# Kernel tuning notes

Hardware: AMD Instinct MI355X
Metric: run time of the kernel (lower is better)

The kernel has to match this reference:

```python
import jax, jax.numpy as jnp
import numpy as np

SIMPLE_W = 1.0
NON_SIMPLE_W = 5.0

# connectivity offset sets (exclude center)
_ALL26 = [(a, b, c) for a in (-1, 0, 1) for b in (-1, 0, 1) for c in (-1, 0, 1) if (a, b, c) != (0, 0, 0)]
OFF6 = [o for o in _ALL26 if abs(o[0]) + abs(o[1]) + abs(o[2]) == 1]          # scipy default structure
OFF18 = [o for o in _ALL26 if not (abs(o[0]) == 1 and abs(o[1]) == 1 and abs(o[2]) == 1)]  # the 's' structure
OFF26 = _ALL26                                                                  # np.ones((3,3,3))


def global_label(fg):
    """Connected-component labels (6-connectivity) via max-propagation.
    Labels are distinct positive ints per component (values differ from scipy's
    1..K but only label *equality* is used downstream). fg: bool [D,H,W]."""
    D, H, W = fg.shape
    idx = (jnp.arange(fg.size, dtype=jnp.int32) + 1).reshape(fg.shape)
    lab0 = jnp.where(fg, idx, 0)

    def step(lab):
        p = jnp.pad(lab, 1)
        m = lab
        for dz, dy, dx in OFF6:
            m = jnp.maximum(m, p[1 + dz:1 + dz + D, 1 + dy:1 + dy + H, 1 + dx:1 + dx + W])
        return jnp.where(fg, m, 0)

    def cond(c):
        return ~c[1]

    def body(c):
        lab, _ = c
        new = step(lab)
        return new, jnp.all(new == lab)

    lab, _ = jax.lax.while_loop(cond, body, (lab0, jnp.array(False)))
    return lab


def local_ncomp(mask, offsets):
    """Number of connected components inside each 3x3x3 window.
    mask: bool [N,3,3,3]. Max-propagation of unique seeds for 26 iters
    (>= max path length among 27 voxels); a component is counted where the
    surviving max label equals its own seed."""
    seed = (jnp.arange(27, dtype=jnp.int32) + 1).reshape(3, 3, 3)
    lab0 = jnp.where(mask, seed, 0)

    def body(_, lab):
        p = jnp.pad(lab, ((0, 0), (1, 1), (1, 1), (1, 1)))
        m = lab
        for dz, dy, dx in offsets:
            m = jnp.maximum(m, p[:, 1 + dz:4 + dz, 1 + dy:4 + dy, 1 + dx:4 + dx])
        return jnp.where(mask, m, 0)

    lab = jax.lax.fori_loop(0, 26, body, lab0)
    return jnp.sum((lab == seed) & mask, axis=(1, 2, 3))


def nonsimple_map(x):
    """Per-voxel non-simple-point indicator, float, same shape as x."""
    D, H, W = x.shape
    fg = x > 0
    glab = global_label(fg)
    p = jnp.pad(glab, 1, mode='edge')  # np.pad(..., 'edge')
    # 3x3x3 label windows per voxel -> [N,3,3,3]
    wins = jnp.stack([p[dz:dz + D, dy:dy + H, dx:dx + W]
                      for dz in range(3) for dy in range(3) for dx in range(3)], axis=-1)
    wins = wins.reshape(-1, 3, 3, 3)
    center = wins[:, 1, 1, 1]  # [N]
    c = center[:, None, None, None]
    # test 1: complement-of-center-label components (18-connectivity) must be exactly 1
    n1 = local_ncomp(wins != c, OFF18)
    # test 2: center-label components with center voxel removed (26-conn) must be exactly 1
    mask2 = (wins == c).at[:, 1, 1, 1].set(False)
    n2 = local_ncomp(mask2, OFF26)
    ns = (center != 0) & ((n1 != 1) | (n2 != 1))
    return ns.reshape(D, H, W).astype(x.dtype)


def setup_inputs() -> dict:
    key = jax.random.key(0)
    k1, k2 = jax.random.split(key)
    D = H = W = 64
    prediction = jax.random.normal(k1, (D, H, W), dtype=jnp.float32)
    label = jax.random.randint(k2, (D, H, W), 0, 2).astype(jnp.float32)
    return {"prediction": prediction, "label": label}


def reference(prediction, label):
    pw = nonsimple_map(prediction)
    lw = nonsimple_map(label)
    w_bool = (pw + lw) > 0
    weight = jnp.where(w_bool, NON_SIMPLE_W, SIMPLE_W).astype(prediction.dtype)
    # BCEWithLogitsLoss(reduction='none'): max(x,0) - x*y + log(1+exp(-|x|))
    cost = jnp.maximum(prediction, 0.0) - prediction * label + jnp.log1p(jnp.exp(-jnp.abs(prediction)))
    return jnp.mean(weight * cost)
```

## Files before the change

kernel.cpp:

```cpp
#include <hip/hip_runtime.h>

#define DIM 64
#define NVOX (DIM * DIM * DIM)
#define EPF 53248

__device__ __forceinline__ int find_root_link(int* L, int v) {
    for (;;) {
        int p = L[v];
        if (p == v) return v;
        int gp = L[p];
        if (gp == p) return p;
        L[v] = gp;
        v = gp;
    }
}

__device__ __forceinline__ void unite(int* L, int a, int b) {
    int ra = find_root_link(L, a);
    int rb = find_root_link(L, b);
    while (ra != rb) {
        if (ra > rb) { int t = ra; ra = rb; rb = t; }
        int old = atomicCAS(&L[rb], rb, ra);
        if (old == rb) break;
        rb = find_root_link(L, old);
        ra = find_root_link(L, ra);
    }
}

__device__ __forceinline__ int chase(const int* __restrict__ L, int p) {
    int q = L[p];
    while (q != p) { p = q; q = L[p]; }
    return p;
}

__global__ void local_ccl(const float* __restrict__ pred,
                          const float* __restrict__ lab,
                          int* __restrict__ LP, int* __restrict__ LL,
                          float* __restrict__ out) {
    __shared__ int s_lab[2048];
    int t = threadIdx.x;
    if (blockIdx.x == 0 && blockIdx.y == 0 && t == 0) *out = 0.0f;
    int b = blockIdx.x;
    int tx = b & 3, ty = (b >> 2) & 3, tz = b >> 4;
    int X0 = tx << 4, Y0 = ty << 4, Z0 = tz << 3;

    const float* src = blockIdx.y ? lab : pred;
    int* Lg = blockIdx.y ? LL : LP;

    bool fg[8];
    int vv[8];
#pragma unroll
    for (int i = 0; i < 8; ++i) {
        int l = t + (i << 8);
        int v = ((Z0 + (l >> 8)) << 12) | ((Y0 + ((l >> 4) & 15)) << 6)
              | (X0 + (l & 15));
        vv[i] = v;
        fg[i] = src[v] > 0.0f;
        s_lab[l] = fg[i] ? l : -1;
    }
    __syncthreads();

#pragma unroll
    for (int i = 0; i < 8; ++i) {
        if (!fg[i]) continue;
        int l = t + (i << 8);
        int lx = l & 15, ly = (l >> 4) & 15, lz = l >> 8;
        if (lx < 15 && s_lab[l + 1]   >= 0) unite(s_lab, l, l + 1);
        if (ly < 15 && s_lab[l + 16]  >= 0) unite(s_lab, l, l + 16);
        if (lz < 7  && s_lab[l + 256] >= 0) unite(s_lab, l, l + 256);
    }
    __syncthreads();

#pragma unroll
    for (int i = 0; i < 8; ++i) {
        int g = -1;
        if (fg[i]) {
            int p = s_lab[t + (i << 8)];
            while (s_lab[p] != p) p = s_lab[p];
            g = ((Z0 + (p >> 8)) << 12) | ((Y0 + ((p >> 4) & 15)) << 6)
              | (X0 + (p & 15));
        }
        Lg[vv[i]] = g;
    }
}

__global__ void boundary_link(int* __restrict__ LP, int* __restrict__ LL) {
    int r = blockIdx.x * blockDim.x + threadIdx.x;
    int v, n;
    if (r < 12288) {
        int plane = 15 + ((r >> 12) << 4);
        int ij = r & 4095;
        v = ((ij >> 6) << 12) | ((ij & 63) << 6) | plane;
        n = v + 1;
    } else if (r < 24576) {
        int r2 = r - 12288;
        int plane = 15 + ((r2 >> 12) << 4);
        int ij = r2 & 4095;
        v = ((ij >> 6) << 12) | (plane << 6) | (ij & 63);
        n = v + 64;
    } else {
        int r3 = r - 24576;
        int plane = 7 + ((r3 >> 12) << 3);
        int ij = r3 & 4095;
        v = (plane << 12) | ((ij >> 6) << 6) | (ij & 63);
        n = v + 4096;
    }

    int lane = threadIdx.x & 63;

    int pa = LP[v], pb = LP[n];
    int la = LL[v], lb = LL[n];
    bool doP = (pa >= 0) & (pb >= 0);
    bool doL = (la >= 0) & (lb >= 0);

    int xpa = __shfl_up(pa, 1, 64), xpb = __shfl_up(pb, 1, 64);
    int xla = __shfl_up(la, 1, 64), xlb = __shfl_up(lb, 1, 64);
    if (lane && xpa == pa && xpb == pb) doP = false;
    if (lane && xla == la && xlb == lb) doL = false;

    int rp0 = -1, rp1 = -1, rl0 = -1, rl1 = -1;
    if (doP) {
        int u0 = chase(LP, pa), u1 = chase(LP, pb);
        rp0 = min(u0, u1); rp1 = max(u0, u1);
    }
    if (doL) {
        int u0 = chase(LL, la), u1 = chase(LL, lb);
        rl0 = min(u0, u1); rl1 = max(u0, u1);
    }

    int qp0 = __shfl_up(rp0, 1, 64), qp1 = __shfl_up(rp1, 1, 64);
    int ql0 = __shfl_up(rl0, 1, 64), ql1 = __shfl_up(rl1, 1, 64);
    bool dupP = lane && (qp0 == rp0) && (qp1 == rp1);
    bool dupL = lane && (ql0 == rl0) && (ql1 == rl1);

    if (rp0 >= 0 && rp0 != rp1 && !dupP) unite(LP, rp0, rp1);
    if (rl0 >= 0 && rl0 != rl1 && !dupL) unite(LL, rl0, rl1);
}

#define MX_L 0x6DB6DB6u
#define MX_R 0x36DB6DBu
#define MY_L 0x7E3F1F8u
#define MY_R 0x0FC7E3Fu
#define M27  0x7FFFFFFu

__device__ __forceinline__ unsigned dil26(unsigned m) {
    m |= ((m << 1) & MX_L) | ((m >> 1) & MX_R);
    m |= ((m << 3) & MY_L) | ((m >> 3) & MY_R);
    m |= ((m << 9) & M27)  | (m >> 9);
    return m;
}
__device__ __forceinline__ unsigned dil18(unsigned m) {
    unsigned ax = m | ((m << 1) & MX_L) | ((m >> 1) & MX_R);
    unsigned ay = m | ((m << 3) & MY_L) | ((m >> 3) & MY_R);
    unsigned dxy = ax | ((ax << 3) & MY_L) | ((ax >> 3) & MY_R);
    unsigned dxz = ax | ((ax << 9) & M27)  | (ax >> 9);
    unsigned dyz = ay | ((ay << 9) & M27)  | (ay >> 9);
    return dxy | dxz | dyz;
}

__device__ __forceinline__ bool single18(unsigned m) {
    if (!m) return false;
    unsigned c = m & (~m + 1u);
    for (;;) {
        unsigned n = dil18(c) & m;
        if (n == m) return true;
        if (n == c) return false;
        c = n;
    }
}
__device__ __forceinline__ bool single26(unsigned m) {
    if (!m) return false;
    unsigned c = m & (~m + 1u);
    for (;;) {
        unsigned n = dil26(c) & m;
        if (n == m) return true;
        if (n == c) return false;
        c = n;
    }
}

#define HV 1000

__global__ void finalize_kernel(const float* __restrict__ pred,
                                const float* __restrict__ lab,
                                const int* __restrict__ LP,
                                const int* __restrict__ LL,
                                float* __restrict__ out) {
    __shared__ int sP[HV], sL[HV];
    __shared__ float s_part[4];
    int t = threadIdx.x;
    int b = blockIdx.x;
    int rx = b & 7, ry = (b >> 3) & 7, rz = b >> 6;
    int x0 = rx << 3, y0 = ry << 3, z0 = rz << 3;

    int pv[4], lv[4];
#pragma unroll
    for (int j = 0; j < 4; ++j) {
        int i = t + (j << 8);
        if (i < HV) {
            int hx = i % 10, rr = i / 10, hy = rr % 10, hz = rr / 10;
            int gx = x0 + hx - 1; gx = gx < 0 ? 0 : (gx > 63 ? 63 : gx);
            int gy = y0 + hy - 1; gy = gy < 0 ? 0 : (gy > 63 ? 63 : gy);
            int gz = z0 + hz - 1; gz = gz < 0 ? 0 : (gz > 63 ? 63 : gz);
            int gv = (gz << 12) | (gy << 6) | gx;
            pv[j] = LP[gv];
            lv[j] = LL[gv];
        }
    }
#pragma unroll
    for (int j = 0; j < 4; ++j) {
        int i = t + (j << 8);
        if (i < HV) {
            int p = pv[j];
            if (p >= 0) p = chase(LP, p);
            sP[i] = p;
            p = lv[j];
            if (p >= 0) p = chase(LL, p);
            sL[i] = p;
        }
    }
    __syncthreads();

    float acc = 0.0f;
#pragma unroll
    for (int j = 0; j < 2; ++j) {
        int l = t + (j << 8);
        int lx = l & 7, ly = (l >> 3) & 7, lz = l >> 6;
        int x = x0 | lx, y = y0 | ly, z = z0 | lz;
        int v = (z << 12) | (y << 6) | x;
        int base = lz * 100 + ly * 10 + lx;

        bool nsP = false, nsL = false;
        {
            int c = sP[base + 111];
            if (c >= 0) {
                unsigned m1 = 0, m2 = 0; int k = 0;
#pragma unroll
                for (int kz = 0; kz < 3; ++kz)
#pragma unroll
                    for (int ky = 0; ky < 3; ++ky)
#pragma unroll
                        for (int kx = 0; kx < 3; ++kx, ++k) {
                            int w = sP[base + kz * 100 + ky * 10 + kx];
                            m1 |= (unsigned)(w != c) << k;
                            m2 |= (unsigned)(w == c) << k;
                        }
                m2 &= ~(1u << 13);
                nsP = !(single18(m1) && single26(m2));
            }
        }
        {
            int c = sL[base + 111];
            if (c >= 0) {
                unsigned m1 = 0, m2 = 0; int k = 0;
#pragma unroll
                for (int kz = 0; kz < 3; ++kz)
#pragma unroll
                    for (int ky = 0; ky < 3; ++ky)
#pragma unroll
                        for (int kx = 0; kx < 3; ++kx, ++k) {
                            int w = sL[base + kz * 100 + ky * 10 + kx];
                            m1 |= (unsigned)(w != c) << k;
                            m2 |= (unsigned)(w == c) << k;
                        }
                m2 &= ~(1u << 13);
                nsL = !(single18(m1) && single26(m2));
            }
        }

        float p = pred[v], lvf = lab[v];
        float cost = fmaxf(p, 0.0f) - p * lvf + log1pf(__expf(-fabsf(p)));
        acc += ((nsP || nsL) ? 5.0f : 1.0f) * cost;
    }

#pragma unroll
    for (int off = 32; off > 0; off >>= 1)
        acc += __shfl_down(acc, off, 64);
    if ((t & 63) == 0) s_part[t >> 6] = acc;
    __syncthreads();
    if (t == 0) {
        float s = s_part[0] + s_part[1] + s_part[2] + s_part[3];
        atomicAdd(out, s * (1.0f / (float)NVOX));
    }
}

extern "C" void kernel_launch(void* const* d_in, const int* in_sizes, int n_in,
                              void* d_out, int out_size, void* d_ws, size_t ws_size,
                              hipStream_t stream) {
    const float* pred = (const float*)d_in[0];
    const float* lab  = (const float*)d_in[1];
    float* out = (float*)d_out;

    int* LP = (int*)d_ws;
    int* LL = LP + NVOX;

    hipLaunchKernelGGL(local_ccl, dim3(128, 2), dim3(256), 0, stream,
                       pred, lab, LP, LL, out);
    hipLaunchKernelGGL(boundary_link, dim3(EPF / 256), dim3(256), 0, stream,
                       LP, LL);
    hipLaunchKernelGGL(finalize_kernel, dim3(512), dim3(256), 0, stream,
                       pred, lab, LP, LL, out);
}
```

Measured before the change: 110.0 us.

## Fuse three CCL kernels into one cooperative kernel with grid syncs

Merges local tile labeling, boundary linking and the finalize/loss pass into a single cooperative launch of 512 blocks, separated by grid-wide barriers, and reuses one shared-memory union for the tile and halo buffers. The local labeling phase also switches to float4/int4 vectorized loads and stores with 4 consecutive voxels per thread. The goal is to remove two kernel launch gaps. In exchange, every phase now runs at 512 blocks, which is idle capacity for the 256-block labeling phase, and it adds grid.sync overhead and a dependence on all blocks being co-resident.

```diff
diff --git a/kernel.cpp b/kernel.cpp
--- a/kernel.cpp
+++ b/kernel.cpp
@@ -1,8 +1,12 @@
 #include <hip/hip_runtime.h>
+#include <hip/hip_cooperative_groups.h>
+
+namespace cg = cooperative_groups;
 
 #define DIM 64
 #define NVOX (DIM * DIM * DIM)
 #define EPF 53248
+#define HV 1000
 
 __device__ __forceinline__ int find_root_link(int* L, int v) {
     for (;;) {
@@ -33,110 +37,6 @@
     return p;
 }
 
-__global__ void local_ccl(const float* __restrict__ pred,
-                          const float* __restrict__ lab,
-                          int* __restrict__ LP, int* __restrict__ LL,
-                          float* __restrict__ out) {
-    __shared__ int s_lab[2048];
-    int t = threadIdx.x;
-    if (blockIdx.x == 0 && blockIdx.y == 0 && t == 0) *out = 0.0f;
-    int b = blockIdx.x;
-    int tx = b & 3, ty = (b >> 2) & 3, tz = b >> 4;
-    int X0 = tx << 4, Y0 = ty << 4, Z0 = tz << 3;
-
-    const float* src = blockIdx.y ? lab : pred;
-    int* Lg = blockIdx.y ? LL : LP;
-
-    bool fg[8];
-    int vv[8];
-#pragma unroll
-    for (int i = 0; i < 8; ++i) {
-        int l = t + (i << 8);
-        int v = ((Z0 + (l >> 8)) << 12) | ((Y0 + ((l >> 4) & 15)) << 6)
-              | (X0 + (l & 15));
-        vv[i] = v;
-        fg[i] = src[v] > 0.0f;
-        s_lab[l] = fg[i] ? l : -1;
-    }
-    __syncthreads();
-
-#pragma unroll
-    for (int i = 0; i < 8; ++i) {
-        if (!fg[i]) continue;
-        int l = t + (i << 8);
-        int lx = l & 15, ly = (l >> 4) & 15, lz = l >> 8;
-        if (lx < 15 && s_lab[l + 1]   >= 0) unite(s_lab, l, l + 1);
-        if (ly < 15 && s_lab[l + 16]  >= 0) unite(s_lab, l, l + 16);
-        if (lz < 7  && s_lab[l + 256] >= 0) unite(s_lab, l, l + 256);
-    }
-    __syncthreads();
-
-#pragma unroll
-    for (int i = 0; i < 8; ++i) {
-        int g = -1;
-        if (fg[i]) {
-            int p = s_lab[t + (i << 8)];
-            while (s_lab[p] != p) p = s_lab[p];
-            g = ((Z0 + (p >> 8)) << 12) | ((Y0 + ((p >> 4) & 15)) << 6)
-              | (X0 + (p & 15));
-        }
-        Lg[vv[i]] = g;
-    }
-}
-
-__global__ void boundary_link(int* __restrict__ LP, int* __restrict__ LL) {
-    int r = blockIdx.x * blockDim.x + threadIdx.x;
-    int v, n;
-    if (r < 12288) {
-        int plane = 15 + ((r >> 12) << 4);
-        int ij = r & 4095;
-        v = ((ij >> 6) << 12) | ((ij & 63) << 6) | plane;
-        n = v + 1;
-    } else if (r < 24576) {
-        int r2 = r - 12288;
-        int plane = 15 + ((r2 >> 12) << 4);
-        int ij = r2 & 4095;
-        v = ((ij >> 6) << 12) | (plane << 6) | (ij & 63);
-        n = v + 64;
-    } else {
-        int r3 = r - 24576;
-        int plane = 7 + ((r3 >> 12) << 3);
-        int ij = r3 & 4095;
-        v = (plane << 12) | ((ij >> 6) << 6) | (ij & 63);
-        n = v + 4096;
-    }
-
-    int lane = threadIdx.x & 63;
-
-    int pa = LP[v], pb = LP[n];
-    int la = LL[v], lb = LL[n];
-    bool doP = (pa >= 0) & (pb >= 0);
-    bool doL = (la >= 0) & (lb >= 0);
-
-    int xpa = __shfl_up(pa, 1, 64), xpb = __shfl_up(pb, 1, 64);
-    int xla = __shfl_up(la, 1, 64), xlb = __shfl_up(lb, 1, 64);
-    if (lane && xpa == pa && xpb == pb) doP = false;
-    if (lane && xla == la && xlb == lb) doL = false;
-
-    int rp0 = -1, rp1 = -1, rl0 = -1, rl1 = -1;
-    if (doP) {
-        int u0 = chase(LP, pa), u1 = chase(LP, pb);
-        rp0 = min(u0, u1); rp1 = max(u0, u1);
-    }
-    if (doL) {
-        int u0 = chase(LL, la), u1 = chase(LL, lb);
-        rl0 = min(u0, u1); rl1 = max(u0, u1);
-    }
-
-    int qp0 = __shfl_up(rp0, 1, 64), qp1 = __shfl_up(rp1, 1, 64);
-    int ql0 = __shfl_up(rl0, 1, 64), ql1 = __shfl_up(rl1, 1, 64);
-    bool dupP = lane && (qp0 == rp0) && (qp1 == rp1);
-    bool dupL = lane && (ql0 == rl0) && (ql1 == rl1);
-
-    if (rp0 >= 0 && rp0 != rp1 && !dupP) unite(LP, rp0, rp1);
-    if (rl0 >= 0 && rl0 != rl1 && !dupL) unite(LL, rl0, rl1);
-}
-
 #define MX_L 0x6DB6DB6u
 #define MX_R 0x36DB6DBu
 #define MY_L 0x7E3F1F8u
@@ -179,108 +79,232 @@
     }
 }
 
-#define HV 1000
-
-__global__ void finalize_kernel(const float* __restrict__ pred,
-                                const float* __restrict__ lab,
-                                const int* __restrict__ LP,
-                                const int* __restrict__ LL,
-                                float* __restrict__ out) {
-    __shared__ int sP[HV], sL[HV];
+__global__ __launch_bounds__(256, 2)
+void fused_all(const float* __restrict__ pred, const float* __restrict__ lab,
+               int* __restrict__ LP, int* __restrict__ LL,
+               float* __restrict__ out) {
+    __shared__ union {
+        int tile[2048];
+        struct { int P[HV]; int L[HV]; } h;
+    } sm;
     __shared__ float s_part[4];
-    int t = threadIdx.x;
-    int b = blockIdx.x;
-    int rx = b & 7, ry = (b >> 3) & 7, rz = b >> 6;
-    int x0 = rx << 3, y0 = ry << 3, z0 = rz << 3;
-
-    int pv[4], lv[4];
-#pragma unroll
-    for (int j = 0; j < 4; ++j) {
-        int i = t + (j << 8);
-        if (i < HV) {
-            int hx = i % 10, rr = i / 10, hy = rr % 10, hz = rr / 10;
-            int gx = x0 + hx - 1; gx = gx < 0 ? 0 : (gx > 63 ? 63 : gx);
-            int gy = y0 + hy - 1; gy = gy < 0 ? 0 : (gy > 63 ? 63 : gy);
-            int gz = z0 + hz - 1; gz = gz < 0 ? 0 : (gz > 63 ? 63 : gz);
-            int gv = (gz << 12) | (gy << 6) | gx;
-            pv[j] = LP[gv];
-            lv[j] = LL[gv];
-        }
-    }
-#pragma unroll
-    for (int j = 0; j < 4; ++j) {
-        int i = t + (j << 8);
-        if (i < HV) {
-            int p = pv[j];
-            if (p >= 0) p = chase(LP, p);
-            sP[i] = p;
-            p = lv[j];
-            if (p >= 0) p = chase(LL, p);
-            sL[i] = p;
-        }
-    }
-    __syncthreads();
-
-    float acc = 0.0f;
-#pragma unroll
-    for (int j = 0; j < 2; ++j) {
-        int l = t + (j << 8);
-        int lx = l & 7, ly = (l >> 3) & 7, lz = l >> 6;
-        int x = x0 | lx, y = y0 | ly, z = z0 | lz;
-        int v = (z << 12) | (y << 6) | x;
-        int base = lz * 100 + ly * 10 + lx;
-
-        bool nsP = false, nsL = false;
-        {
-            int c = sP[base + 111];
-            if (c >= 0) {
-                unsigned m1 = 0, m2 = 0; int k = 0;
-#pragma unroll
-                for (int kz = 0; kz < 3; ++kz)
-#pragma unroll
-                    for (int ky = 0; ky < 3; ++ky)
-#pragma unroll
-                        for (int kx = 0; kx < 3; ++kx, ++k) {
-                            int w = sP[base + kz * 100 + ky * 10 + kx];
-                            m1 |= (unsigned)(w != c) << k;
-                            m2 |= (unsigned)(w == c) << k;
-                        }
-                m2 &= ~(1u << 13);
-                nsP = !(single18(m1) && single26(m2));
-            }
-        }
-        {
-            int c = sL[base + 111];
-            if (c >= 0) {
-                unsigned m1 = 0, m2 = 0; int k = 0;
-#pragma unroll
-                for (int kz = 0; kz < 3; ++kz)
-#pragma unroll
-                    for (int ky = 0; ky < 3; ++ky)
-#pragma unroll
-                        for (int kx = 0; kx < 3; ++kx, ++k) {
-                            int w = sL[base + kz * 100 + ky * 10 + kx];
-                            m1 |= (unsigned)(w != c) << k;
-                            m2 |= (unsigned)(w == c) << k;
-                        }
-                m2 &= ~(1u << 13);
-                nsL = !(single18(m1) && single26(m2));
-            }
-        }
-
-        float p = pred[v], lvf = lab[v];
-        float cost = fmaxf(p, 0.0f) - p * lvf + log1pf(__expf(-fabsf(p)));
-        acc += ((nsP || nsL) ? 5.0f : 1.0f) * cost;
-    }
-
-#pragma unroll
-    for (int off = 32; off > 0; off >>= 1)
-        acc += __shfl_down(acc, off, 64);
-    if ((t & 63) == 0) s_part[t >> 6] = acc;
-    __syncthreads();
-    if (t == 0) {
-        float s = s_part[0] + s_part[1] + s_part[2] + s_part[3];
-        atomicAdd(out, s * (1.0f / (float)NVOX));
+
+    cg::grid_group grid = cg::this_grid();
+    const int t = threadIdx.x;
+    const int b = blockIdx.x;
+
+    if (b == 0 && t == 0) *out = 0.0f;
+
+    if (b < 256) {
+        int tile = b & 127, field = b >> 7;
+        int tx = tile & 3, ty = (tile >> 2) & 3, tz = tile >> 4;
+        int X0 = tx << 4, Y0 = ty << 4, Z0 = tz << 3;
+        const float* src = field ? lab : pred;
+        int* Lg = field ? LL : LP;
+
+        bool fg[8];
+        int vbase[2];
+#pragma unroll
+        for (int j = 0; j < 2; ++j) {
+            int l0 = (j << 10) | (t << 2);
+            int lx = l0 & 15, ly = (l0 >> 4) & 15, lz = l0 >> 8;
+            int v0 = ((Z0 + lz) << 12) | ((Y0 + ly) << 6) | (X0 + lx);
+            vbase[j] = v0;
+            const float4 f = *reinterpret_cast<const float4*>(src + v0);
+            int4 s;
+            fg[j * 4 + 0] = f.x > 0.0f; s.x = fg[j * 4 + 0] ? l0 + 0 : -1;
+            fg[j * 4 + 1] = f.y > 0.0f; s.y = fg[j * 4 + 1] ? l0 + 1 : -1;
+            fg[j * 4 + 2] = f.z > 0.0f; s.z = fg[j * 4 + 2] ? l0 + 2 : -1;
+            fg[j * 4 + 3] = f.w > 0.0f; s.w = fg[j * 4 + 3] ? l0 + 3 : -1;
+            *reinterpret_cast<int4*>(&sm.tile[l0]) = s;
+        }
+        __syncthreads();
+
+#pragma unroll
+        for (int j = 0; j < 2; ++j) {
+#pragma unroll
+            for (int k = 0; k < 4; ++k) {
+                if (!fg[j * 4 + k]) continue;
+                int l = ((j << 10) | (t << 2)) + k;
+                int lx = l & 15, ly = (l >> 4) & 15, lz = l >> 8;
+                if (lx < 15 && sm.tile[l + 1]   >= 0) unite(sm.tile, l, l + 1);
+                if (ly < 15 && sm.tile[l + 16]  >= 0) unite(sm.tile, l, l + 16);
+                if (lz < 7  && sm.tile[l + 256] >= 0) unite(sm.tile, l, l + 256);
+            }
+        }
+        __syncthreads();
+
+#pragma unroll
+        for (int j = 0; j < 2; ++j) {
+            int l0 = (j << 10) | (t << 2);
+            int rr[4];
+#pragma unroll
+            for (int k = 0; k < 4; ++k) {
+                int g = -1;
+                if (fg[j * 4 + k]) {
+                    int p = sm.tile[l0 + k];
+                    while (sm.tile[p] != p) p = sm.tile[p];
+                    g = ((Z0 + (p >> 8)) << 12) | ((Y0 + ((p >> 4) & 15)) << 6)
+                      | (X0 + (p & 15));
+                }
+                rr[k] = g;
+            }
+            *reinterpret_cast<int4*>(Lg + vbase[j]) =
+                make_int4(rr[0], rr[1], rr[2], rr[3]);
+        }
+    }
+
+    grid.sync();
+
+    {
+        int e = (b << 8) | t;
+        if (e < EPF) {
+            int v, n;
+            if (e < 12288) {
+                int plane = 15 + ((e >> 12) << 4);
+                int ij = e & 4095;
+                v = ((ij >> 6) << 12) | ((ij & 63) << 6) | plane;
+                n = v + 1;
+            } else if (e < 24576) {
+                int e2 = e - 12288;
+                int plane = 15 + ((e2 >> 12) << 4);
+                int ij = e2 & 4095;
+                v = ((ij >> 6) << 12) | (plane << 6) | (ij & 63);
+                n = v + 64;
+            } else {
+                int e3 = e - 24576;
+                int plane = 7 + ((e3 >> 12) << 3);
+                int ij = e3 & 4095;
+                v = (plane << 12) | ((ij >> 6) << 6) | (ij & 63);
+                n = v + 4096;
+            }
+
+            int lane = t & 63;
+            int pa = LP[v], pb = LP[n];
+            int la = LL[v], lb = LL[n];
+            bool doP = (pa >= 0) & (pb >= 0);
+            bool doL = (la >= 0) & (lb >= 0);
+
+            int xpa = __shfl_up(pa, 1, 64), xpb = __shfl_up(pb, 1, 64);
+            int xla = __shfl_up(la, 1, 64), xlb = __shfl_up(lb, 1, 64);
+            if (lane && xpa == pa && xpb == pb) doP = false;
+            if (lane && xla == la && xlb == lb) doL = false;
+
+            int rp0 = -1, rp1 = -1, rl0 = -1, rl1 = -1;
+            if (doP) {
+                int u0 = chase(LP, pa), u1 = chase(LP, pb);
+                rp0 = min(u0, u1); rp1 = max(u0, u1);
+            }
+            if (doL) {
+                int u0 = chase(LL, la), u1 = chase(LL, lb);
+                rl0 = min(u0, u1); rl1 = max(u0, u1);
+            }
+
+            int qp0 = __shfl_up(rp0, 1, 64), qp1 = __shfl_up(rp1, 1, 64);
+            int ql0 = __shfl_up(rl0, 1, 64), ql1 = __shfl_up(rl1, 1, 64);
+            bool dupP = lane && (qp0 == rp0) && (qp1 == rp1);
+            bool dupL = lane && (ql0 == rl0) && (ql1 == rl1);
+
+            if (rp0 >= 0 && rp0 != rp1 && !dupP) unite(LP, rp0, rp1);
+            if (rl0 >= 0 && rl0 != rl1 && !dupL) unite(LL, rl0, rl1);
+        }
+    }
+
+    grid.sync();
+
+    {
+        int rx = b & 7, ry = (b >> 3) & 7, rz = b >> 6;
+        int x0 = rx << 3, y0 = ry << 3, z0 = rz << 3;
+
+        int pv[4], lv[4];
+#pragma unroll
+        for (int j = 0; j < 4; ++j) {
+            int i = t + (j << 8);
+            if (i < HV) {
+                int hx = i % 10, rr = i / 10, hy = rr % 10, hz = rr / 10;
+                int gx = x0 + hx - 1; gx = gx < 0 ? 0 : (gx > 63 ? 63 : gx);
+                int gy = y0 + hy - 1; gy = gy < 0 ? 0 : (gy > 63 ? 63 : gy);
+                int gz = z0 + hz - 1; gz = gz < 0 ? 0 : (gz > 63 ? 63 : gz);
+                int gv = (gz << 12) | (gy << 6) | gx;
+                pv[j] = LP[gv];
+                lv[j] = LL[gv];
+            }
+        }
+#pragma unroll
+        for (int j = 0; j < 4; ++j) {
+            int i = t + (j << 8);
+            if (i < HV) {
+                int p = pv[j];
+                if (p >= 0) p = chase(LP, p);
+                sm.h.P[i] = p;
+                p = lv[j];
+                if (p >= 0) p = chase(LL, p);
+                sm.h.L[i] = p;
+            }
+        }
+        __syncthreads();
+
+        float acc = 0.0f;
+#pragma unroll
+        for (int j = 0; j < 2; ++j) {
+            int l = t + (j << 8);
+            int lx = l & 7, ly = (l >> 3) & 7, lz = l >> 6;
+            int x = x0 | lx, y = y0 | ly, z = z0 | lz;
+            int v = (z << 12) | (y << 6) | x;
+            int base = lz * 100 + ly * 10 + lx;
+
+            bool nsP = false, nsL = false;
+            {
+                int c = sm.h.P[base + 111];
+                if (c >= 0) {
+                    unsigned m1 = 0, m2 = 0; int k = 0;
+#pragma unroll
+                    for (int kz = 0; kz < 3; ++kz)
+#pragma unroll
+                        for (int ky = 0; ky < 3; ++ky)
+#pragma unroll
+                            for (int kx = 0; kx < 3; ++kx, ++k) {
+                                int w = sm.h.P[base + kz * 100 + ky * 10 + kx];
+                                m1 |= (unsigned)(w != c) << k;
+                                m2 |= (unsigned)(w == c) << k;
+                            }
+                    m2 &= ~(1u << 13);
+                    nsP = !(single18(m1) && single26(m2));
+                }
+            }
+            {
+                int c = sm.h.L[base + 111];
+                if (c >= 0) {
+                    unsigned m1 = 0, m2 = 0; int k = 0;
+#pragma unroll
+                    for (int kz = 0; kz < 3; ++kz)
+#pragma unroll
+                        for (int ky = 0; ky < 3; ++ky)
+#pragma unroll
+                            for (int kx = 0; kx < 3; ++kx, ++k) {
+                                int w = sm.h.L[base + kz * 100 + ky * 10 + kx];
+                                m1 |= (unsigned)(w != c) << k;
+                                m2 |= (unsigned)(w == c) << k;
+                            }
+                    m2 &= ~(1u << 13);
+                    nsL = !(single18(m1) && single26(m2));
+                }
+            }
+
+            float p = pred[v], lvf = lab[v];
+            float cost = fmaxf(p, 0.0f) - p * lvf + log1pf(__expf(-fabsf(p)));
+            acc += ((nsP || nsL) ? 5.0f : 1.0f) * cost;
+        }
+
+#pragma unroll
+        for (int off = 32; off > 0; off >>= 1)
+            acc += __shfl_down(acc, off, 64);
+        if ((t & 63) == 0) s_part[t >> 6] = acc;
+        __syncthreads();
+        if (t == 0) {
+            float s = s_part[0] + s_part[1] + s_part[2] + s_part[3];
+            atomicAdd(out, s * (1.0f / (float)NVOX));
+        }
     }
 }
 
@@ -294,10 +318,8 @@
     int* LP = (int*)d_ws;
     int* LL = LP + NVOX;
 
-    hipLaunchKernelGGL(local_ccl, dim3(128, 2), dim3(256), 0, stream,
-                       pred, lab, LP, LL, out);
-    hipLaunchKernelGGL(boundary_link, dim3(EPF / 256), dim3(256), 0, stream,
-                       LP, LL);
-    hipLaunchKernelGGL(finalize_kernel, dim3(512), dim3(256), 0, stream,
-                       pred, lab, LP, LL, out);
-}
+    void* args[] = { (void*)&pred, (void*)&lab, (void*)&LP, (void*)&LL,
+                     (void*)&out };
+    hipLaunchCooperativeKernel((const void*)fused_all, dim3(512), dim3(256),
+                               args, 0, stream);
+}
```

Result: slower. 222.5 us (+102.3%).

## Add flatten pass, vectorize local CCL, halve finalize tile depth

Applied to the files above, without the earlier changes.

Local CCL now runs 512 threads per block, each handling 4 consecutive voxels with float4 loads and int4 stores instead of 8 strided voxels. A new flatten kernel compresses every union-find label to its root once, so finalize no longer chases roots for its halo. Finalize uses 8x8x4 tiles (600-entry halo, 1024 blocks, one voxel per thread) to raise parallelism. The cost is an extra kernel launch and a full pass over both label arrays, plus more redundant halo loads overall.

```diff
diff --git a/kernel.cpp b/kernel.cpp
--- a/kernel.cpp
+++ b/kernel.cpp
@@ -33,10 +33,11 @@
     return p;
 }
 
-__global__ void local_ccl(const float* __restrict__ pred,
-                          const float* __restrict__ lab,
-                          int* __restrict__ LP, int* __restrict__ LL,
-                          float* __restrict__ out) {
+__global__ __launch_bounds__(512)
+void local_ccl(const float* __restrict__ pred,
+               const float* __restrict__ lab,
+               int* __restrict__ LP, int* __restrict__ LL,
+               float* __restrict__ out) {
     __shared__ int s_lab[2048];
     int t = threadIdx.x;
     if (blockIdx.x == 0 && blockIdx.y == 0 && t == 0) *out = 0.0f;
@@ -47,23 +48,26 @@
     const float* src = blockIdx.y ? lab : pred;
     int* Lg = blockIdx.y ? LL : LP;
 
-    bool fg[8];
-    int vv[8];
-#pragma unroll
-    for (int i = 0; i < 8; ++i) {
-        int l = t + (i << 8);
-        int v = ((Z0 + (l >> 8)) << 12) | ((Y0 + ((l >> 4) & 15)) << 6)
-              | (X0 + (l & 15));
-        vv[i] = v;
-        fg[i] = src[v] > 0.0f;
-        s_lab[l] = fg[i] ? l : -1;
+    int l0 = t << 2;
+    int lx0 = l0 & 15, ly0 = (l0 >> 4) & 15, lz0 = l0 >> 8;
+    int v0 = ((Z0 + lz0) << 12) | ((Y0 + ly0) << 6) | (X0 + lx0);
+
+    bool fg[4];
+    {
+        const float4 f = *reinterpret_cast<const float4*>(src + v0);
+        int4 s;
+        fg[0] = f.x > 0.0f; s.x = fg[0] ? l0 + 0 : -1;
+        fg[1] = f.y > 0.0f; s.y = fg[1] ? l0 + 1 : -1;
+        fg[2] = f.z > 0.0f; s.z = fg[2] ? l0 + 2 : -1;
+        fg[3] = f.w > 0.0f; s.w = fg[3] ? l0 + 3 : -1;
+        *reinterpret_cast<int4*>(&s_lab[l0]) = s;
     }
     __syncthreads();
 
 #pragma unroll
-    for (int i = 0; i < 8; ++i) {
-        if (!fg[i]) continue;
-        int l = t + (i << 8);
+    for (int k = 0; k < 4; ++k) {
+        if (!fg[k]) continue;
+        int l = l0 + k;
         int lx = l & 15, ly = (l >> 4) & 15, lz = l >> 8;
         if (lx < 15 && s_lab[l + 1]   >= 0) unite(s_lab, l, l + 1);
         if (ly < 15 && s_lab[l + 16]  >= 0) unite(s_lab, l, l + 16);
@@ -71,20 +75,25 @@
     }
     __syncthreads();
 
-#pragma unroll
-    for (int i = 0; i < 8; ++i) {
-        int g = -1;
-        if (fg[i]) {
-            int p = s_lab[t + (i << 8)];
-            while (s_lab[p] != p) p = s_lab[p];
-            g = ((Z0 + (p >> 8)) << 12) | ((Y0 + ((p >> 4) & 15)) << 6)
-              | (X0 + (p & 15));
-        }
-        Lg[vv[i]] = g;
-    }
-}
-
-__global__ void boundary_link(int* __restrict__ LP, int* __restrict__ LL) {
+    {
+        int rr[4];
+#pragma unroll
+        for (int k = 0; k < 4; ++k) {
+            int g = -1;
+            if (fg[k]) {
+                int p = s_lab[l0 + k];
+                while (s_lab[p] != p) p = s_lab[p];
+                g = ((Z0 + (p >> 8)) << 12) | ((Y0 + ((p >> 4) & 15)) << 6)
+                  | (X0 + (p & 15));
+            }
+            rr[k] = g;
+        }
+        *reinterpret_cast<int4*>(Lg + v0) = make_int4(rr[0], rr[1], rr[2], rr[3]);
+    }
+}
+
+__global__ __launch_bounds__(256)
+void boundary_link(int* __restrict__ LP, int* __restrict__ LL) {
     int r = blockIdx.x * blockDim.x + threadIdx.x;
     int v, n;
     if (r < 12288) {
@@ -137,6 +146,18 @@
     if (rl0 >= 0 && rl0 != rl1 && !dupL) unite(LL, rl0, rl1);
 }
 
+__global__ __launch_bounds__(256)
+void flatten(int* __restrict__ LP, int* __restrict__ LL) {
+    int idx = blockIdx.x * blockDim.x + threadIdx.x;
+    int* L = (idx < NVOX) ? LP : LL;
+    int i = idx & (NVOX - 1);
+    int p = L[i];
+    if (p >= 0) {
+        int r = chase(L, p);
+        if (r != p) L[i] = r;
+    }
+}
+
 #define MX_L 0x6DB6DB6u
 #define MX_R 0x36DB6DBu
 #define MY_L 0x7E3F1F8u
@@ -179,25 +200,26 @@
     }
 }
 
-#define HV 1000
-
-__global__ void finalize_kernel(const float* __restrict__ pred,
-                                const float* __restrict__ lab,
-                                const int* __restrict__ LP,
-                                const int* __restrict__ LL,
-                                float* __restrict__ out) {
-    __shared__ int sP[HV], sL[HV];
+#define HV2 600
+
+__global__ __launch_bounds__(256, 4)
+void finalize_kernel(const float* __restrict__ pred,
+                     const float* __restrict__ lab,
+                     const int* __restrict__ LP,
+                     const int* __restrict__ LL,
+                     float* __restrict__ out) {
+    __shared__ int sP[HV2], sL[HV2];
     __shared__ float s_part[4];
     int t = threadIdx.x;
     int b = blockIdx.x;
     int rx = b & 7, ry = (b >> 3) & 7, rz = b >> 6;
-    int x0 = rx << 3, y0 = ry << 3, z0 = rz << 3;
-
-    int pv[4], lv[4];
-#pragma unroll
-    for (int j = 0; j < 4; ++j) {
+    int x0 = rx << 3, y0 = ry << 3, z0 = rz << 2;
+
+    int pv[3], lv[3];
+#pragma unroll
+    for (int j = 0; j < 3; ++j) {
         int i = t + (j << 8);
-        if (i < HV) {
+        if (i < HV2) {
             int hx = i % 10, rr = i / 10, hy = rr % 10, hz = rr / 10;
             int gx = x0 + hx - 1; gx = gx < 0 ? 0 : (gx > 63 ? 63 : gx);
             int gy = y0 + hy - 1; gy = gy < 0 ? 0 : (gy > 63 ? 63 : gy);
@@ -208,23 +230,18 @@
         }
     }
 #pragma unroll
-    for (int j = 0; j < 4; ++j) {
+    for (int j = 0; j < 3; ++j) {
         int i = t + (j << 8);
-        if (i < HV) {
-            int p = pv[j];
-            if (p >= 0) p = chase(LP, p);
-            sP[i] = p;
-            p = lv[j];
-            if (p >= 0) p = chase(LL, p);
-            sL[i] = p;
+        if (i < HV2) {
+            sP[i] = pv[j];
+            sL[i] = lv[j];
         }
     }
     __syncthreads();
 
-    float acc = 0.0f;
-#pragma unroll
-    for (int j = 0; j < 2; ++j) {
-        int l = t + (j << 8);
+    float acc;
+    {
+        int l = t;
         int lx = l & 7, ly = (l >> 3) & 7, lz = l >> 6;
         int x = x0 | lx, y = y0 | ly, z = z0 | lz;
         int v = (z << 12) | (y << 6) | x;
@@ -270,7 +287,7 @@
 
         float p = pred[v], lvf = lab[v];
         float cost = fmaxf(p, 0.0f) - p * lvf + log1pf(__expf(-fabsf(p)));
-        acc += ((nsP || nsL) ? 5.0f : 1.0f) * cost;
+        acc = ((nsP || nsL) ? 5.0f : 1.0f) * cost;
     }
 
 #pragma unroll
@@ -294,10 +311,12 @@
     int* LP = (int*)d_ws;
     int* LL = LP + NVOX;
 
-    hipLaunchKernelGGL(local_ccl, dim3(128, 2), dim3(256), 0, stream,
+    hipLaunchKernelGGL(local_ccl, dim3(128, 2), dim3(512), 0, stream,
                        pred, lab, LP, LL, out);
     hipLaunchKernelGGL(boundary_link, dim3(EPF / 256), dim3(256), 0, stream,
                        LP, LL);
-    hipLaunchKernelGGL(finalize_kernel, dim3(512), dim3(256), 0, stream,
+    hipLaunchKernelGGL(flatten, dim3(2 * NVOX / 256), dim3(256), 0, stream,
+                       LP, LL);
+    hipLaunchKernelGGL(finalize_kernel, dim3(1024), dim3(256), 0, stream,
                        pred, lab, LP, LL, out);
 }
```

Measured after the change: 109.2 us. Within noise of the previous version (-0.7%).
